# Kernel tuning notes

Measured on AMD Instinct MI355X. Metric: run time of the kernel, lower is better.

## Reference

```python
import jax, jax.numpy as jnp
import numpy as np

N_NODES = 50000
N_EDGES = 800000
NUM_GRAPHS = 64
D_IN = 128
D_HID = 128
D_OUT = 1
SLOPE = 0.01  # default leaky_relu negative slope


def setup_inputs() -> dict:
    key = jax.random.key(0)
    ks = jax.random.split(key, 8)
    x = jax.random.normal(ks[0], (N_NODES, D_IN), dtype=jnp.float32)
    edge_index = jax.random.randint(ks[1], (2, N_EDGES), 0, N_NODES, dtype=jnp.int64)
    batch = jnp.sort(jax.random.randint(ks[2], (N_NODES,), 0, NUM_GRAPHS, dtype=jnp.int64))
    s_in = 1.0 / np.sqrt(D_IN)
    s_h = 1.0 / np.sqrt(D_HID)
    W0 = jax.random.uniform(ks[3], (D_IN, D_HID), jnp.float32, -s_in, s_in)
    W1 = jax.random.uniform(ks[4], (D_HID, D_HID), jnp.float32, -s_h, s_h)
    W2 = jax.random.uniform(ks[5], (D_HID, D_HID), jnp.float32, -s_h, s_h)
    Wfc1 = jax.random.uniform(ks[6], (D_HID, D_HID), jnp.float32, -s_h, s_h)
    Wfc2 = jax.random.uniform(ks[7], (D_HID, D_OUT), jnp.float32, -s_h, s_h)
    return {"x": x, "edge_index": edge_index, "batch": batch,
            "W0": W0, "W1": W1, "W2": W2, "Wfc1": Wfc1, "Wfc2": Wfc2}


def _leaky(v):
    return jnp.where(v >= 0, v, SLOPE * v)


def _gcn_layer(x, row, col, dinv, W):
    # GCNConv: h = x W; out = D^-1/2 (A+I) D^-1/2 h  (unit edge weights)
    h = x @ W
    coef = (dinv[row] * dinv[col])[:, None]            # [E,1]
    agg = jax.ops.segment_sum(h[row] * coef, col, num_segments=N_NODES)
    return agg + h * (dinv * dinv)[:, None]            # self-loop term


def reference(x, edge_index, batch, W0, W1, W2, Wfc1, Wfc2):
    row, col = edge_index[0], edge_index[1]
    # degree with self loops (edge weight 1); same for all layers
    deg = jax.ops.segment_sum(jnp.ones(N_EDGES, x.dtype), col, num_segments=N_NODES) + 1.0
    dinv = jax.lax.rsqrt(deg)
    h = x
    for W in (W0, W1, W2):
        h = _leaky(_gcn_layer(h, row, col, dinv, W))
    y = _leaky(h @ Wfc1)
    y = _leaky(y @ Wfc2)                               # [N, 1]
    # avg_pool_x(batch, y, batch): mean of y per graph id
    sums = jax.ops.segment_sum(y, batch, num_segments=NUM_GRAPHS)
    cnts = jax.ops.segment_sum(jnp.ones(N_NODES, y.dtype), batch, num_segments=NUM_GRAPHS)
    return sums / jnp.maximum(cnts, 1.0)[:, None]      # [NUM_GRAPHS, 1]
```

## Files before the change

### kernel.cpp

```cpp
#include <hip/hip_runtime.h>

#define N_NODES   50000
#define N_EDGES   800000
#define NUM_GRAPHS 64
#define D         128
#define SLOPE     0.01

__device__ __forceinline__ double dleaky(double v) { return v >= 0.0 ? v : SLOPE * v; }

__global__ void zero_kernel(int* __restrict__ p, int n) {
    int i = blockIdx.x * blockDim.x + threadIdx.x;
    if (i < n) p[i] = 0;
}

__global__ void hist_kernel(const int* __restrict__ col, int* __restrict__ hist, int E) {
    int e = blockIdx.x * blockDim.x + threadIdx.x;
    if (e < E) atomicAdd(&hist[col[e]], 1);
}

__global__ void dinv_kernel(const int* __restrict__ hist, double* __restrict__ dinvd, int n) {
    int i = blockIdx.x * blockDim.x + threadIdx.x;
    if (i < n) dinvd[i] = 1.0 / sqrt((double)hist[i] + 1.0);
}

__global__ __launch_bounds__(256) void scan1(const int* __restrict__ hist,
                                             int* __restrict__ start,
                                             int* __restrict__ bsum, int n) {
    __shared__ int tmp[256];
    const int tid = threadIdx.x;
    int base = blockIdx.x * 1024 + tid * 4;
    int v[4]; int s = 0;
#pragma unroll
    for (int i = 0; i < 4; ++i) { int idx = base + i; v[i] = (idx < n) ? hist[idx] : 0; s += v[i]; }
    tmp[tid] = s;
    __syncthreads();
    for (int off = 1; off < 256; off <<= 1) {
        int t = (tid >= off) ? tmp[tid - off] : 0;
        __syncthreads();
        tmp[tid] += t;
        __syncthreads();
    }
    int run = tmp[tid] - s;
    if (tid == 255) bsum[blockIdx.x] = tmp[255];
#pragma unroll
    for (int i = 0; i < 4; ++i) { int idx = base + i; if (idx < n) start[idx] = run; run += v[i]; }
}

__global__ __launch_bounds__(256) void scan2(int* __restrict__ bsum, int nb,
                                             int* __restrict__ start, int n) {
    __shared__ int tmp[256];
    const int tid = threadIdx.x;
    int v = (tid < nb) ? bsum[tid] : 0;
    tmp[tid] = v;
    __syncthreads();
    for (int off = 1; off < 256; off <<= 1) {
        int t = (tid >= off) ? tmp[tid - off] : 0;
        __syncthreads();
        tmp[tid] += t;
        __syncthreads();
    }
    if (tid < nb) bsum[tid] = tmp[tid] - v;
    if (tid == 255) start[n] = tmp[255];
}

__global__ __launch_bounds__(256) void scan3(int* __restrict__ start, int* __restrict__ cursor,
                                             const int* __restrict__ bsum, int n) {
    int off = bsum[blockIdx.x];
    int base = blockIdx.x * 1024 + threadIdx.x * 4;
#pragma unroll
    for (int i = 0; i < 4; ++i) {
        int j = base + i;
        if (j < n) { int v = start[j] + off; start[j] = v; cursor[j] = v; }
    }
}

__global__ void build_kernel(const int* __restrict__ row, const int* __restrict__ col,
                             int* __restrict__ cursor, int* __restrict__ srcrow, int E) {
    int e = blockIdx.x * blockDim.x + threadIdx.x;
    if (e >= E) return;
    int p = atomicAdd(&cursor[col[e]], 1);
    srcrow[p] = row[e];
}

__global__ void gbound_kernel(const int* __restrict__ batch, int* __restrict__ gstart, int n) {
    int i = blockIdx.x * blockDim.x + threadIdx.x;
    if (i >= n) return;
    int b = batch[i];
    int prev = (i == 0) ? -1 : batch[i - 1];
    for (int g = prev + 1; g <= b; ++g) gstart[g] = i;
    if (i == n - 1) {
        for (int g = b + 1; g <= NUM_GRAPHS; ++g) gstart[g] = n;
    }
}

__global__ __launch_bounds__(256, 4) void gemm128_d(const float* __restrict__ A,
                                                    const float* __restrict__ W,
                                                    float* __restrict__ C, int M, int act,
                                                    const double* __restrict__ scale) {
    __shared__ double As[64][33];
    __shared__ float  Ws[32][129];
    const int tid = threadIdx.x;
    const int rg = tid >> 4;
    const int cg = tid & 15;
    const int rowBase = blockIdx.x * 64;

    double acc[4][8];
#pragma unroll
    for (int r = 0; r < 4; ++r)
#pragma unroll
        for (int j = 0; j < 8; ++j) acc[r][j] = 0.0;

    const int lr = tid >> 2;
    const int lc = (tid & 3) * 8;
    const int wr = tid & 31;
    const int wc = (tid >> 5) * 16;

    const int growA = rowBase + lr;
    const bool haveA = (growA < M);

    float4 a0 = make_float4(0.f, 0.f, 0.f, 0.f), a1 = a0;
    if (haveA) {
        const float4* src = reinterpret_cast<const float4*>(A + (size_t)growA * D + 0 + lc);
        a0 = src[0]; a1 = src[1];
    }

    for (int kc = 0; kc < 128; kc += 32) {
        *reinterpret_cast<double2*>(&As[lr][lc + 0]) = make_double2((double)a0.x, (double)a0.y);
        *reinterpret_cast<double2*>(&As[lr][lc + 2]) = make_double2((double)a0.z, (double)a0.w);
        *reinterpret_cast<double2*>(&As[lr][lc + 4]) = make_double2((double)a1.x, (double)a1.y);
        *reinterpret_cast<double2*>(&As[lr][lc + 6]) = make_double2((double)a1.z, (double)a1.w);
        {
            const float4* src = reinterpret_cast<const float4*>(W + (size_t)(kc + wr) * D + wc);
#pragma unroll
            for (int i = 0; i < 4; ++i)
                *reinterpret_cast<float4*>(&Ws[wr][wc + 4 * i]) = src[i];
        }
        __syncthreads();

        if (kc + 32 < 128 && haveA) {
            const float4* src = reinterpret_cast<const float4*>(A + (size_t)growA * D + (kc + 32) + lc);
            a0 = src[0]; a1 = src[1];
        }

#pragma unroll
        for (int k = 0; k < 32; ++k) {
            double xv0 = As[rg * 4 + 0][k];
            double xv1 = As[rg * 4 + 1][k];
            double xv2 = As[rg * 4 + 2][k];
            double xv3 = As[rg * 4 + 3][k];
            double w0 = (double)Ws[k][cg +   0];
            double w1 = (double)Ws[k][cg +  16];
            double w2 = (double)Ws[k][cg +  32];
            double w3 = (double)Ws[k][cg +  48];
            double w4 = (double)Ws[k][cg +  64];
            double w5 = (double)Ws[k][cg +  80];
            double w6 = (double)Ws[k][cg +  96];
            double w7 = (double)Ws[k][cg + 112];
            acc[0][0] = fma(xv0, w0, acc[0][0]); acc[0][1] = fma(xv0, w1, acc[0][1]);
            acc[0][2] = fma(xv0, w2, acc[0][2]); acc[0][3] = fma(xv0, w3, acc[0][3]);
            acc[0][4] = fma(xv0, w4, acc[0][4]); acc[0][5] = fma(xv0, w5, acc[0][5]);
            acc[0][6] = fma(xv0, w6, acc[0][6]); acc[0][7] = fma(xv0, w7, acc[0][7]);
            acc[1][0] = fma(xv1, w0, acc[1][0]); acc[1][1] = fma(xv1, w1, acc[1][1]);
            acc[1][2] = fma(xv1, w2, acc[1][2]); acc[1][3] = fma(xv1, w3, acc[1][3]);
            acc[1][4] = fma(xv1, w4, acc[1][4]); acc[1][5] = fma(xv1, w5, acc[1][5]);
            acc[1][6] = fma(xv1, w6, acc[1][6]); acc[1][7] = fma(xv1, w7, acc[1][7]);
            acc[2][0] = fma(xv2, w0, acc[2][0]); acc[2][1] = fma(xv2, w1, acc[2][1]);
            acc[2][2] = fma(xv2, w2, acc[2][2]); acc[2][3] = fma(xv2, w3, acc[2][3]);
            acc[2][4] = fma(xv2, w4, acc[2][4]); acc[2][5] = fma(xv2, w5, acc[2][5]);
            acc[2][6] = fma(xv2, w6, acc[2][6]); acc[2][7] = fma(xv2, w7, acc[2][7]);
            acc[3][0] = fma(xv3, w0, acc[3][0]); acc[3][1] = fma(xv3, w1, acc[3][1]);
            acc[3][2] = fma(xv3, w2, acc[3][2]); acc[3][3] = fma(xv3, w3, acc[3][3]);
            acc[3][4] = fma(xv3, w4, acc[3][4]); acc[3][5] = fma(xv3, w5, acc[3][5]);
            acc[3][6] = fma(xv3, w6, acc[3][6]); acc[3][7] = fma(xv3, w7, acc[3][7]);
        }
        __syncthreads();
    }

#pragma unroll
    for (int r = 0; r < 4; ++r) {
        int grow = rowBase + rg * 4 + r;
        if (grow < M) {
            double sc = scale ? scale[grow] : 1.0;
#pragma unroll
            for (int j = 0; j < 8; ++j) {
                double v = acc[r][j];
                if (act) v = dleaky(v);
                v *= sc;
                C[(size_t)grow * D + cg + 16 * j] = (float)v;
            }
        }
    }
}

__global__ __launch_bounds__(256) void agg_s(const float* __restrict__ hp,
                                             const int* __restrict__ srcrow,
                                             const int* __restrict__ start,
                                             const double* __restrict__ dinvd,
                                             float* __restrict__ out, int n) {
    int node = (int)((blockIdx.x * blockDim.x + threadIdx.x) >> 6);
    int lane = threadIdx.x & 63;
    if (node >= n) return;
    int s = start[node], e = start[node + 1];
    double dn = dinvd[node];
    const int f = lane * 2;
    float2 hs = *reinterpret_cast<const float2*>(hp + (size_t)node * D + f);
    double ax = 0.0, ay = 0.0;
    int p = s;
    for (; p + 16 <= e; p += 16) {
        int r[16]; float2 hv[16];
#pragma unroll
        for (int i = 0; i < 16; ++i) r[i] = srcrow[p + i];
#pragma unroll
        for (int i = 0; i < 16; ++i)
            hv[i] = *reinterpret_cast<const float2*>(hp + (size_t)r[i] * D + f);
#pragma unroll
        for (int i = 0; i < 16; ++i) { ax += (double)hv[i].x; ay += (double)hv[i].y; }
    }
    for (; p + 8 <= e; p += 8) {
        int r[8]; float2 hv[8];
#pragma unroll
        for (int i = 0; i < 8; ++i) r[i] = srcrow[p + i];
#pragma unroll
        for (int i = 0; i < 8; ++i)
            hv[i] = *reinterpret_cast<const float2*>(hp + (size_t)r[i] * D + f);
#pragma unroll
        for (int i = 0; i < 8; ++i) { ax += (double)hv[i].x; ay += (double)hv[i].y; }
    }
    for (; p < e; ++p) {
        int r = srcrow[p];
        float2 hv = *reinterpret_cast<const float2*>(hp + (size_t)r * D + f);
        ax += (double)hv.x; ay += (double)hv.y;
    }
    ax = dleaky((ax + (double)hs.x) * dn);
    ay = dleaky((ay + (double)hs.y) * dn);
    *reinterpret_cast<float2*>(out + (size_t)node * D + f) =
        make_float2((float)ax, (float)ay);
}

__global__ __launch_bounds__(256) void fc2_d(const float* __restrict__ y,
                                             const float* __restrict__ w,
                                             double* __restrict__ s, int n) {
    int node = (int)((blockIdx.x * blockDim.x + threadIdx.x) >> 6);
    int lane = threadIdx.x & 63;
    if (node >= n) return;
    float2 yv = *reinterpret_cast<const float2*>(y + (size_t)node * D + lane * 2);
    float2 wv = *reinterpret_cast<const float2*>(w + lane * 2);
    double part = (double)yv.x * (double)wv.x + (double)yv.y * (double)wv.y;
#pragma unroll
    for (int off = 32; off > 0; off >>= 1) part += __shfl_down(part, off, 64);
    if (lane == 0) s[node] = dleaky(part);
}

__global__ __launch_bounds__(256) void pool2(const double* __restrict__ s,
                                             const int* __restrict__ gstart,
                                             float* __restrict__ out) {
    __shared__ double lsum[256];
    const int g = blockIdx.x;
    const int tid = threadIdx.x;
    const int s0 = gstart[g], s1 = gstart[g + 1];
    double sum = 0.0;
    for (int i = s0 + tid; i < s1; i += 256) sum += s[i];
    lsum[tid] = sum;
    __syncthreads();
    for (int off = 128; off > 0; off >>= 1) {
        if (tid < off) lsum[tid] += lsum[tid + off];
        __syncthreads();
    }
    if (tid == 0) {
        int cnt = s1 - s0;
        out[g] = (float)(lsum[0] / (double)(cnt > 0 ? cnt : 1));
    }
}

extern "C" void kernel_launch(void* const* d_in, const int* in_sizes, int n_in,
                              void* d_out, int out_size, void* d_ws, size_t ws_size,
                              hipStream_t stream) {
    const float* x    = (const float*)d_in[0];
    const int*   eidx = (const int*)d_in[1];
    const int*   batch= (const int*)d_in[2];
    const float* W0   = (const float*)d_in[3];
    const float* W1   = (const float*)d_in[4];
    const float* W2   = (const float*)d_in[5];
    const float* Wfc1 = (const float*)d_in[6];
    const float* Wfc2 = (const float*)d_in[7];
    float* out = (float*)d_out;

    const int* erow = eidx;
    const int* ecol = eidx + N_EDGES;

    char* ws = (char*)d_ws;
    int*    hist   = (int*)   (ws + 0);
    int*    start  = (int*)   (ws + 200064);
    int*    cursor = (int*)   (ws + 400384);
    int*    bsum   = (int*)   (ws + 600448);
    double* dinvd  = (double*)(ws + 600704);
    int*    srcrow = (int*)   (ws + 1000704);
    double* svec   = (double*)(ws + 4200704);
    float*  bufA   = (float*) (ws + 4600832);
    float*  bufB   = (float*) (ws + 30200832);
    int*    gstart = cursor;

    zero_kernel<<<(N_NODES + 255) / 256, 256, 0, stream>>>(hist, N_NODES);
    hist_kernel<<<(N_EDGES + 255) / 256, 256, 0, stream>>>(ecol, hist, N_EDGES);
    dinv_kernel<<<(N_NODES + 255) / 256, 256, 0, stream>>>(hist, dinvd, N_NODES);

    const int NB = (N_NODES + 1023) / 1024;
    scan1<<<NB, 256, 0, stream>>>(hist, start, bsum, N_NODES);
    scan2<<<1, 256, 0, stream>>>(bsum, NB, start, N_NODES);
    scan3<<<NB, 256, 0, stream>>>(start, cursor, bsum, N_NODES);

    build_kernel<<<(N_EDGES + 255) / 256, 256, 0, stream>>>(erow, ecol, cursor, srcrow, N_EDGES);
    gbound_kernel<<<(N_NODES + 255) / 256, 256, 0, stream>>>(batch, gstart, N_NODES);

    const int GEMM_GRID = (N_NODES + 63) / 64;
    const int AGG_GRID  = (N_NODES + 3) / 4;

    gemm128_d<<<GEMM_GRID, 256, 0, stream>>>(x, W0, bufA, N_NODES, 0, dinvd);
    agg_s<<<AGG_GRID, 256, 0, stream>>>(bufA, srcrow, start, dinvd, bufB, N_NODES);
    gemm128_d<<<GEMM_GRID, 256, 0, stream>>>(bufB, W1, bufA, N_NODES, 0, dinvd);
    agg_s<<<AGG_GRID, 256, 0, stream>>>(bufA, srcrow, start, dinvd, bufB, N_NODES);
    gemm128_d<<<GEMM_GRID, 256, 0, stream>>>(bufB, W2, bufA, N_NODES, 0, dinvd);
    agg_s<<<AGG_GRID, 256, 0, stream>>>(bufA, srcrow, start, dinvd, bufB, N_NODES);
    gemm128_d<<<GEMM_GRID, 256, 0, stream>>>(bufB, Wfc1, bufA, N_NODES, 1, (const double*)nullptr);

    fc2_d<<<AGG_GRID, 256, 0, stream>>>(bufA, Wfc2, svec, N_NODES);
    pool2<<<NUM_GRAPHS, 256, 0, stream>>>(svec, gstart, out);
}
```

Baseline: 500.3 us.

## Use FP64 MFMA 16x16x4 instructions in the 128-wide GEMM kernel

Replaces the scalar FP64 FMA register-tiled GEMM with one built on the matrix-core FP64 MFMA intrinsic. Each of the four waves computes a 16x64 output tile through four accumulators, and the block row tile shrinks from 64 to 32 rows, which doubles the grid. This moves the double-precision matmul work from the vector ALUs to the matrix units. The trade-off is less A-tile reuse per block and more blocks and W reloads.

```diff
diff --git a/kernel.cpp b/kernel.cpp
--- a/kernel.cpp
+++ b/kernel.cpp
@@ -5,6 +5,8 @@
 #define NUM_GRAPHS 64
 #define D         128
 #define SLOPE     0.01
+
+typedef double d4 __attribute__((ext_vector_type(4)));
 
 __device__ __forceinline__ double dleaky(double v) { return v >= 0.0 ? v : SLOPE * v; }
 
@@ -93,42 +95,44 @@
     }
 }
 
-__global__ __launch_bounds__(256, 4) void gemm128_d(const float* __restrict__ A,
-                                                    const float* __restrict__ W,
-                                                    float* __restrict__ C, int M, int act,
-                                                    const double* __restrict__ scale) {
-    __shared__ double As[64][33];
+__global__ __launch_bounds__(256, 4) void gemm128_mfma(const float* __restrict__ A,
+                                                       const float* __restrict__ W,
+                                                       float* __restrict__ C, int M, int act,
+                                                       const double* __restrict__ scale) {
+    __shared__ double As[32][33];
     __shared__ float  Ws[32][129];
-    const int tid = threadIdx.x;
-    const int rg = tid >> 4;
-    const int cg = tid & 15;
-    const int rowBase = blockIdx.x * 64;
-
-    double acc[4][8];
-#pragma unroll
-    for (int r = 0; r < 4; ++r)
-#pragma unroll
-        for (int j = 0; j < 8; ++j) acc[r][j] = 0.0;
-
-    const int lr = tid >> 2;
-    const int lc = (tid & 3) * 8;
+    const int tid  = threadIdx.x;
+    const int lane = tid & 63;
+    const int wid  = tid >> 6;
+    const int wrow = wid >> 1;
+    const int wcol = wid & 1;
+    const int rowBase = blockIdx.x * 32;
+
+    d4 acc0 = {0.0, 0.0, 0.0, 0.0};
+    d4 acc1 = {0.0, 0.0, 0.0, 0.0};
+    d4 acc2 = {0.0, 0.0, 0.0, 0.0};
+    d4 acc3 = {0.0, 0.0, 0.0, 0.0};
+
+    const int lr = tid >> 3;
+    const int lc = (tid & 7) * 4;
     const int wr = tid & 31;
     const int wc = (tid >> 5) * 16;
 
     const int growA = rowBase + lr;
     const bool haveA = (growA < M);
 
-    float4 a0 = make_float4(0.f, 0.f, 0.f, 0.f), a1 = a0;
-    if (haveA) {
-        const float4* src = reinterpret_cast<const float4*>(A + (size_t)growA * D + 0 + lc);
-        a0 = src[0]; a1 = src[1];
-    }
+    float4 a0 = make_float4(0.f, 0.f, 0.f, 0.f);
+    if (haveA) a0 = *reinterpret_cast<const float4*>(A + (size_t)growA * D + lc);
+
+    const int arow = wrow * 16 + (lane & 15);
+    const int asub = lane >> 4;
+    const int bcol = wcol * 64 + (lane & 15);
 
     for (int kc = 0; kc < 128; kc += 32) {
-        *reinterpret_cast<double2*>(&As[lr][lc + 0]) = make_double2((double)a0.x, (double)a0.y);
-        *reinterpret_cast<double2*>(&As[lr][lc + 2]) = make_double2((double)a0.z, (double)a0.w);
-        *reinterpret_cast<double2*>(&As[lr][lc + 4]) = make_double2((double)a1.x, (double)a1.y);
-        *reinterpret_cast<double2*>(&As[lr][lc + 6]) = make_double2((double)a1.z, (double)a1.w);
+        As[lr][lc + 0] = (double)a0.x;
+        As[lr][lc + 1] = (double)a0.y;
+        As[lr][lc + 2] = (double)a0.z;
+        As[lr][lc + 3] = (double)a0.w;
         {
             const float4* src = reinterpret_cast<const float4*>(W + (size_t)(kc + wr) * D + wc);
 #pragma unroll
@@ -137,57 +141,39 @@
         }
         __syncthreads();
 
-        if (kc + 32 < 128 && haveA) {
-            const float4* src = reinterpret_cast<const float4*>(A + (size_t)growA * D + (kc + 32) + lc);
-            a0 = src[0]; a1 = src[1];
+        if (kc + 32 < 128 && haveA)
+            a0 = *reinterpret_cast<const float4*>(A + (size_t)growA * D + (kc + 32) + lc);
+
+#pragma unroll
+        for (int kk = 0; kk < 8; ++kk) {
+            double av = As[arow][kk * 4 + asub];
+            double b0 = (double)Ws[kk * 4 + asub][bcol +  0];
+            double b1 = (double)Ws[kk * 4 + asub][bcol + 16];
+            double b2 = (double)Ws[kk * 4 + asub][bcol + 32];
+            double b3 = (double)Ws[kk * 4 + asub][bcol + 48];
+            acc0 = __builtin_amdgcn_mfma_f64_16x16x4f64(av, b0, acc0, 0, 0, 0);
+            acc1 = __builtin_amdgcn_mfma_f64_16x16x4f64(av, b1, acc1, 0, 0, 0);
+            acc2 = __builtin_amdgcn_mfma_f64_16x16x4f64(av, b2, acc2, 0, 0, 0);
+            acc3 = __builtin_amdgcn_mfma_f64_16x16x4f64(av, b3, acc3, 0, 0, 0);
         }
-
-#pragma unroll
-        for (int k = 0; k < 32; ++k) {
-            double xv0 = As[rg * 4 + 0][k];
-            double xv1 = As[rg * 4 + 1][k];
-            double xv2 = As[rg * 4 + 2][k];
-            double xv3 = As[rg * 4 + 3][k];
-            double w0 = (double)Ws[k][cg +   0];
-            double w1 = (double)Ws[k][cg +  16];
-            double w2 = (double)Ws[k][cg +  32];
-            double w3 = (double)Ws[k][cg +  48];
-            double w4 = (double)Ws[k][cg +  64];
-            double w5 = (double)Ws[k][cg +  80];
-            double w6 = (double)Ws[k][cg +  96];
-            double w7 = (double)Ws[k][cg + 112];
-            acc[0][0] = fma(xv0, w0, acc[0][0]); acc[0][1] = fma(xv0, w1, acc[0][1]);
-            acc[0][2] = fma(xv0, w2, acc[0][2]); acc[0][3] = fma(xv0, w3, acc[0][3]);
-            acc[0][4] = fma(xv0, w4, acc[0][4]); acc[0][5] = fma(xv0, w5, acc[0][5]);
-            acc[0][6] = fma(xv0, w6, acc[0][6]); acc[0][7] = fma(xv0, w7, acc[0][7]);
-            acc[1][0] = fma(xv1, w0, acc[1][0]); acc[1][1] = fma(xv1, w1, acc[1][1]);
-            acc[1][2] = fma(xv1, w2, acc[1][2]); acc[1][3] = fma(xv1, w3, acc[1][3]);
-            acc[1][4] = fma(xv1, w4, acc[1][4]); acc[1][5] = fma(xv1, w5, acc[1][5]);
-            acc[1][6] = fma(xv1, w6, acc[1][6]); acc[1][7] = fma(xv1, w7, acc[1][7]);
-            acc[2][0] = fma(xv2, w0, acc[2][0]); acc[2][1] = fma(xv2, w1, acc[2][1]);
-            acc[2][2] = fma(xv2, w2, acc[2][2]); acc[2][3] = fma(xv2, w3, acc[2][3]);
-            acc[2][4] = fma(xv2, w4, acc[2][4]); acc[2][5] = fma(xv2, w5, acc[2][5]);
-            acc[2][6] = fma(xv2, w6, acc[2][6]); acc[2][7] = fma(xv2, w7, acc[2][7]);
-            acc[3][0] = fma(xv3, w0, acc[3][0]); acc[3][1] = fma(xv3, w1, acc[3][1]);
-            acc[3][2] = fma(xv3, w2, acc[3][2]); acc[3][3] = fma(xv3, w3, acc[3][3]);
-            acc[3][4] = fma(xv3, w4, acc[3][4]); acc[3][5] = fma(xv3, w5, acc[3][5]);
-            acc[3][6] = fma(xv3, w6, acc[3][6]); acc[3][7] = fma(xv3, w7, acc[3][7]);
-        }
-        __syncthreads();
-    }
-
+        __syncthreads();
+    }
+
+    const int rbase = rowBase + wrow * 16 + 4 * (lane >> 4);
+    const int cb = wcol * 64 + (lane & 15);
 #pragma unroll
     for (int r = 0; r < 4; ++r) {
-        int grow = rowBase + rg * 4 + r;
+        int grow = rbase + r;
         if (grow < M) {
             double sc = scale ? scale[grow] : 1.0;
-#pragma unroll
-            for (int j = 0; j < 8; ++j) {
-                double v = acc[r][j];
-                if (act) v = dleaky(v);
-                v *= sc;
-                C[(size_t)grow * D + cg + 16 * j] = (float)v;
-            }
+            double v0 = acc0[r], v1 = acc1[r], v2 = acc2[r], v3 = acc3[r];
+            if (act) { v0 = dleaky(v0); v1 = dleaky(v1); v2 = dleaky(v2); v3 = dleaky(v3); }
+            v0 *= sc; v1 *= sc; v2 *= sc; v3 *= sc;
+            float* crow = C + (size_t)grow * D + cb;
+            crow[ 0] = (float)v0;
+            crow[16] = (float)v1;
+            crow[32] = (float)v2;
+            crow[48] = (float)v3;
         }
     }
 }
@@ -312,16 +298,16 @@
     build_kernel<<<(N_EDGES + 255) / 256, 256, 0, stream>>>(erow, ecol, cursor, srcrow, N_EDGES);
     gbound_kernel<<<(N_NODES + 255) / 256, 256, 0, stream>>>(batch, gstart, N_NODES);
 
-    const int GEMM_GRID = (N_NODES + 63) / 64;
+    const int GEMM_GRID = (N_NODES + 31) / 32;
     const int AGG_GRID  = (N_NODES + 3) / 4;
 
-    gemm128_d<<<GEMM_GRID, 256, 0, stream>>>(x, W0, bufA, N_NODES, 0, dinvd);
+    gemm128_mfma<<<GEMM_GRID, 256, 0, stream>>>(x, W0, bufA, N_NODES, 0, dinvd);
     agg_s<<<AGG_GRID, 256, 0, stream>>>(bufA, srcrow, start, dinvd, bufB, N_NODES);
-    gemm128_d<<<GEMM_GRID, 256, 0, stream>>>(bufB, W1, bufA, N_NODES, 0, dinvd);
+    gemm128_mfma<<<GEMM_GRID, 256, 0, stream>>>(bufB, W1, bufA, N_NODES, 0, dinvd);
     agg_s<<<AGG_GRID, 256, 0, stream>>>(bufA, srcrow, start, dinvd, bufB, N_NODES);
-    gemm128_d<<<GEMM_GRID, 256, 0, stream>>>(bufB, W2, bufA, N_NODES, 0, dinvd);
+    gemm128_mfma<<<GEMM_GRID, 256, 0, stream>>>(bufB, W2, bufA, N_NODES, 0, dinvd);
     agg_s<<<AGG_GRID, 256, 0, stream>>>(bufA, srcrow, start, dinvd, bufB, N_NODES);
-    gemm128_d<<<GEMM_GRID, 256, 0, stream>>>(bufB, Wfc1, bufA, N_NODES, 1, (const double*)nullptr);
+    gemm128_mfma<<<GEMM_GRID, 256, 0, stream>>>(bufB, Wfc1, bufA, N_NODES, 1, (const double*)nullptr);
 
     fc2_d<<<AGG_GRID, 256, 0, stream>>>(bufA, Wfc2, svec, N_NODES);
     pool2<<<NUM_GRAPHS, 256, 0, stream>>>(svec, gstart, out);
```

After: 465.3 us. 1.08x faster.
